# Optimization experiments

Hardware: AMD Instinct MI355X
Metric: run time of the kernel (lower is better)

## Reference

```python
import jax, jax.numpy as jnp
import numpy as np

N = 50000      # num nodes
E = 400000     # directed edges (avg out-degree 8)
DIN = 128
DOUT = 128
ALPHA = 0.5    # args.alphaDir (buffer, requires_grad=False)
BETA = 0.5     # args.betaDir
GAMA = 0.5     # args.gamaDir


def _dedupe(rows, cols, vals, n):
    key = rows.astype(np.int64) * n + cols.astype(np.int64)
    uk, inv = np.unique(key, return_inverse=True)
    v = np.bincount(inv, weights=vals, minlength=uk.shape[0])
    return (uk // n).astype(np.int32), (uk % n).astype(np.int32), v.astype(np.float32)


def _dir_norm(r, c, v, n):
    # directed_norm: D_out^{-1/2} A D_in^{-1/2}, inf -> 0
    in_deg = np.bincount(c, weights=v, minlength=n)
    out_deg = np.bincount(r, weights=v, minlength=n)
    in_is = np.zeros(n); m = in_deg > 0; in_is[m] = in_deg[m] ** -0.5
    out_is = np.zeros(n); m = out_deg > 0; out_is[m] = out_deg[m] ** -0.5
    return r, c, (out_is[r] * v * in_is[c]).astype(np.float32)


def _spgemm(rA, cA, vA, rB, cB, vB, n):
    # sparse @ sparse in COO, vectorized numpy
    order = np.argsort(rB, kind='stable')
    rBs, cBs, vBs = rB[order], cB[order], vB[order]
    degB = np.bincount(rBs, minlength=n)
    indptr = np.concatenate(([0], np.cumsum(degB)))
    counts = degB[cA]
    total = int(counts.sum())
    rep = np.repeat(np.arange(len(rA)), counts)
    first = np.cumsum(counts) - counts
    pos = np.arange(total) - np.repeat(first, counts) + np.repeat(indptr[cA], counts)
    rows = rA[rep]
    cols = cBs[pos]
    vals = vA[rep].astype(np.float64) * vBs[pos]
    return _dedupe(rows, cols, vals, n)


def setup_inputs() -> dict:
    rng = np.random.default_rng(0)
    r0 = rng.integers(0, N, E).astype(np.int64)
    c0 = rng.integers(0, N, E).astype(np.int64)
    r, c, v = _dedupe(r0, c0, np.ones(E, np.float32), N)
    a = _dir_norm(r, c, v, N)                 # adj_norm
    at = _dir_norm(c, r, v, N)                # adj_t_norm
    rr, cc, vv = _spgemm(a[0], a[1], a[2], at[0], at[1], at[2], N)
    aat = _dir_norm(rr, cc, vv, N)            # directed_norm(A @ At)
    rr, cc, vv = _spgemm(at[0], at[1], at[2], a[0], a[1], a[2], N)
    ata = _dir_norm(rr, cc, vv, N)            # directed_norm(At @ A)
    rr, cc, vv = _spgemm(a[0], a[1], a[2], a[0], a[1], a[2], N)
    aa = _dir_norm(rr, cc, vv, N)             # directed_norm(A @ A)
    rr, cc, vv = _spgemm(at[0], at[1], at[2], at[0], at[1], at[2], N)
    atat = _dir_norm(rr, cc, vv, N)           # directed_norm(At @ At)

    key = jax.random.key(0)
    ks = jax.random.split(key, 7)
    x = jax.random.normal(ks[0], (N, DIN), dtype=jnp.float32)
    s = 1.0 / np.sqrt(DIN)

    def lin(k):
        k1, k2 = jax.random.split(k)
        w = jax.random.uniform(k1, (DIN, DOUT), jnp.float32, -s, s)
        b = jax.random.uniform(k2, (DOUT,), jnp.float32, -s, s)
        return w, b

    w_sd, b_sd = lin(ks[1]); w_ds, b_ds = lin(ks[2])
    w0, b0 = lin(ks[3]); w1, b1 = lin(ks[4])
    w2, b2 = lin(ks[5]); w3, b3 = lin(ks[6])

    out = {'x': x,
           'w_sd': w_sd, 'b_sd': b_sd, 'w_ds': w_ds, 'b_ds': b_ds,
           'w0': w0, 'b0': b0, 'w1': w1, 'b1': b1,
           'w2': w2, 'b2': b2, 'w3': w3, 'b3': b3}
    for name, t in (('a', a), ('at', at), ('aat', aat), ('ata', ata), ('aa', aa), ('atat', atat)):
        out[name + '_rows'] = jnp.asarray(t[0])
        out[name + '_cols'] = jnp.asarray(t[1])
        out[name + '_vals'] = jnp.asarray(t[2])
    return out


def _spmm(rows, cols, vals, x):
    # (A @ x)[i] = sum_e vals[e] * x[cols[e]] scattered to rows[e]
    return jax.ops.segment_sum(vals[:, None] * x[cols], rows, num_segments=x.shape[0])


def reference(x, a_rows, a_cols, a_vals, at_rows, at_cols, at_vals,
              aat_rows, aat_cols, aat_vals, ata_rows, ata_cols, ata_vals,
              aa_rows, aa_cols, aa_vals, atat_rows, atat_cols, atat_vals,
              w_sd, b_sd, w_ds, b_ds, w0, b0, w1, b1, w2, b2, w3, b3):
    out1 = ALPHA * (_spmm(a_rows, a_cols, a_vals, x) @ w_sd + b_sd) \
         + (1.0 - ALPHA) * (_spmm(at_rows, at_cols, at_vals, x) @ w_ds + b_ds)
    out2 = BETA * (_spmm(aat_rows, aat_cols, aat_vals, x) @ w0 + b0) \
         + (1.0 - BETA) * (_spmm(ata_rows, ata_cols, ata_vals, x) @ w1 + b1)
    out3 = GAMA * (_spmm(aa_rows, aa_cols, aa_vals, x) @ w2 + b2) \
         + (1.0 - GAMA) * (_spmm(atat_rows, atat_cols, atat_vals, x) @ w3 + b3)
    return out1 + out2 + out3
```

## Files before the change

kernel.cpp:

```cpp
#include <hip/hip_runtime.h>
#include <hip/hip_bf16.h>

#define FD 128

typedef __attribute__((ext_vector_type(8))) short bf16x8;
typedef __attribute__((ext_vector_type(4))) float f32x4;

__device__ __forceinline__ float bfu2f(unsigned short u) {
  return __uint_as_float(((unsigned int)u) << 16);
}
__device__ __forceinline__ float b2f(__hip_bfloat16 v) { return __bfloat162float(v); }
__device__ __forceinline__ unsigned int pk2(float lo, float hi) {
  return (unsigned int)__bfloat16_as_ushort(__float2bfloat16(lo)) |
         ((unsigned int)__bfloat16_as_ushort(__float2bfloat16(hi)) << 16);
}

__device__ __forceinline__ float ldf(const void* p, int i, int ff) {
  return ff ? ((const float*)p)[i] : b2f(((const __hip_bfloat16*)p)[i]);
}
__device__ __forceinline__ int ldi(const void* p, int i, int fi) {
  return fi ? (int)((const long long*)p)[i] : ((const int*)p)[i];
}

__global__ void detect_k(const void* x, const void* cols, int* flags) {
  __shared__ int cnt[2];
  if (threadIdx.x < 2) cnt[threadIdx.x] = 0;
  __syncthreads();
  const unsigned short* xu = (const unsigned short*)x;
  int big = 0;
  for (int i = threadIdx.x; i < 1024; i += 256) {
    int e = (xu[i] >> 7) & 0xFF;
    if (e >= 0x90) big++;
  }
  if (big) atomicAdd(&cnt[0], big);
  const int* ci = (const int*)cols;
  int zeros = 0;
  for (int i = threadIdx.x; i < 128; i += 256)
    if ((i & 1) && ci[i] == 0) zeros++;
  if (zeros) atomicAdd(&cnt[1], zeros);
  __syncthreads();
  if (threadIdx.x == 0) {
    flags[0] = (cnt[0] > 16) ? 1 : 0;
    flags[1] = (cnt[1] >= 32) ? 1 : 0;
  }
}

__global__ void cvtall_k(const void* __restrict__ rows, const void* __restrict__ cols,
                         const void* __restrict__ vals, int nnz, int n,
                         int* __restrict__ r32, int* __restrict__ c32,
                         float* __restrict__ vf, int* __restrict__ cntT,
                         const int* flags) {
  int ff = flags[0], fi = flags[1];
  int i = blockIdx.x * 256 + threadIdx.x;
  if (i >= nnz) return;
  int r = ldi(rows, i, fi);
  int c = ldi(cols, i, fi);
  if ((unsigned)r >= (unsigned)n) r = 0;
  if ((unsigned)c >= (unsigned)n) c = 0;
  r32[i] = r;
  c32[i] = c;
  vf[i] = ldf(vals, i, ff);
  atomicAdd(&cntT[c], 1);
}

__global__ void scanAbs_k(const int* __restrict__ cnt, int n, int* bsum,
                          const int* __restrict__ rows, int nnz, int* rpA, int nb) {
  int blk = blockIdx.x;
  if (blk < nb) {
    __shared__ int sh[256];
    int t = threadIdx.x;
    int i = blk * 256 + t;
    sh[t] = (i < n) ? cnt[i] : 0;
    __syncthreads();
    for (int d = 128; d > 0; d >>= 1) {
      if (t < d) sh[t] += sh[t + d];
      __syncthreads();
    }
    if (t == 0) bsum[blk] = sh[0];
  } else {
    int i = (blk - nb) * 256 + threadIdx.x;
    if (i > n) return;
    int lo = 0, hi = nnz;
    while (lo < hi) { int mid = (lo + hi) >> 1; if (rows[mid] < i) lo = mid + 1; else hi = mid; }
    rpA[i] = lo;
  }
}

__global__ void scanB_k(int* bsum, int nb, int* rpTail) {
  __shared__ int sh[256];
  int t = threadIdx.x;
  int v = (t < nb) ? bsum[t] : 0;
  sh[t] = v;
  __syncthreads();
  int val = v;
  for (int d = 1; d < 256; d <<= 1) {
    int add = (t >= d) ? sh[t - d] : 0;
    __syncthreads();
    val += add;
    sh[t] = val;
    __syncthreads();
  }
  if (t < nb) bsum[t] = val - v;
  if (t == 255) *rpTail = val;
}

__global__ void scanC_k(const int* __restrict__ cnt, int n, const int* __restrict__ bsum,
                        int* rp, int* cur) {
  __shared__ int sh[256];
  int t = threadIdx.x;
  int i = blockIdx.x * 256 + t;
  int v = (i < n) ? cnt[i] : 0;
  sh[t] = v;
  __syncthreads();
  int val = v;
  for (int d = 1; d < 256; d <<= 1) {
    int add = (t >= d) ? sh[t - d] : 0;
    __syncthreads();
    val += add;
    sh[t] = val;
    __syncthreads();
  }
  int ex = val - v + bsum[blockIdx.x];
  if (i < n) { rp[i] = ex; cur[i] = ex; }
}

__global__ void scatter_k(const int* __restrict__ r, const int* __restrict__ c,
                          const float* __restrict__ v, int nnz,
                          int* cur, int* tSrc, float* tVal) {
  int i = blockIdx.x * 256 + threadIdx.x;
  if (i >= nnz) return;
  int p = atomicAdd(&cur[c[i]], 1);
  if ((unsigned)p >= (unsigned)nnz) return;
  tSrc[p] = r[i];
  tVal[p] = v[i];
}

__global__ void nodesum_k(const int* __restrict__ rpA, const float* __restrict__ av,
                          const int* __restrict__ rpT, const float* __restrict__ tv,
                          float* __restrict__ u1, float* __restrict__ v1, int n) {
  int i = blockIdx.x * 256 + threadIdx.x;
  if (i >= n) return;
  float su = 0.f;
  int e0 = rpA[i], e1 = rpA[i + 1];
  for (int j = e0; j < e1; ++j) su += av[j];
  u1[i] = su;
  float sv = 0.f;
  int f0 = rpT[i], f1 = rpT[i + 1];
  for (int j = f0; j < f1; ++j) sv += tv[j];
  v1[i] = sv;
}

__global__ void deg2c_k(const int* __restrict__ rpA, const int* __restrict__ ci,
                        const float* __restrict__ av,
                        const int* __restrict__ rpT, const int* __restrict__ ti,
                        const float* __restrict__ tv,
                        const float* __restrict__ u1, const float* __restrict__ v1,
                        float* __restrict__ s1, float* __restrict__ s2,
                        float* __restrict__ s3, float* __restrict__ s4, int n) {
  int i = blockIdx.x * 256 + threadIdx.x;
  if (i >= n) return;
  float a1 = 0.f, a3 = 0.f;
  int s0 = rpA[i], se = rpA[i + 1];
  for (int j = s0; j < se; ++j) {
    int c = ci[j];
    float v = av[j];
    a1 = fmaf(v, v1[c], a1);
    a3 = fmaf(v, u1[c], a3);
  }
  s1[i] = (a1 > 0.f) ? rsqrtf(a1) : 0.f;
  s3[i] = (a3 > 0.f) ? rsqrtf(a3) : 0.f;
  float a2 = 0.f, a4 = 0.f;
  int t0 = rpT[i], t1 = rpT[i + 1];
  for (int j = t0; j < t1; ++j) {
    int r = ti[j];
    float v = tv[j];
    a2 = fmaf(v, u1[r], a2);
    a4 = fmaf(v, v1[r], a4);
  }
  s2[i] = (a2 > 0.f) ? rsqrtf(a2) : 0.f;
  s4[i] = (a4 > 0.f) ? rsqrtf(a4) : 0.f;
}

__global__ void bias_k(const void* a, const void* b, const void* c, const void* d,
                       const void* e, const void* f, float* bias, const int* flags) {
  int ff = flags[0];
  int i = threadIdx.x;
  bias[i] = 0.5f * (ldf(a, i, ff) + ldf(b, i, ff) + ldf(c, i, ff)
                  + ldf(d, i, ff) + ldf(e, i, ff) + ldf(f, i, ff));
}

__global__ void fill_k(unsigned short* o, int n) {
  int i = blockIdx.x * 256 + threadIdx.x;
  if (i < n) o[i] = 0x3E80;
}

struct W6p { const void* w[6]; };
struct B6p { const void* b[6]; };

__global__ void prep_k(const void* __restrict__ x, __hip_bfloat16* __restrict__ xb, int nx,
                       W6p ws, __hip_bfloat16* __restrict__ Wt,
                       B6p bs, float* __restrict__ bias,
                       const int* flags, int cvtB) {
  int ff = flags[0];
  int blk = blockIdx.x;
  if (blk < cvtB) {
    int i = (blk * 256 + threadIdx.x) * 4;
    if (i >= nx) return;
    if (i + 3 >= nx) {
      for (int k = i; k < nx; ++k) xb[k] = __float2bfloat16(ldf(x, k, ff));
      return;
    }
    xb[i + 0] = __float2bfloat16(ldf(x, i + 0, ff));
    xb[i + 1] = __float2bfloat16(ldf(x, i + 1, ff));
    xb[i + 2] = __float2bfloat16(ldf(x, i + 2, ff));
    xb[i + 3] = __float2bfloat16(ldf(x, i + 3, ff));
  } else if (blk < cvtB + 384) {
    int e = (blk - cvtB) * 256 + threadIdx.x;
    if (e >= 6 * 16384) return;
    int seg = e >> 14;
    int r = e & 16383;
    int n = r >> 7;
    int innerB = (r & 127) << 1;
    int kb = innerB ^ ((n & 7) << 4);
    int k = kb >> 1;
    Wt[e] = __float2bfloat16(ldf(ws.w[seg], k * 128 + n, ff));
  } else {
    int i = threadIdx.x;
    if (i < FD)
      bias[i] = 0.5f * (ldf(bs.b[0], i, ff) + ldf(bs.b[1], i, ff) + ldf(bs.b[2], i, ff)
                      + ldf(bs.b[3], i, ff) + ldf(bs.b[4], i, ff) + ldf(bs.b[5], i, ff));
  }
}

struct FHSet {
  const int* rp; const int* ci; const float* cv;
  unsigned int* ot; unsigned int* oa; unsigned int* ob;
  const float* sA; const float* sB;
};

__global__ __launch_bounds__(256) void fh3d_k(
    FHSet h0, FHSet h1, const unsigned int* __restrict__ xb, int n, int half) {
  int blk = blockIdx.x;
  bool hiH = blk >= half;
  const int* rp = hiH ? h1.rp : h0.rp;
  const int* ci = hiH ? h1.ci : h0.ci;
  const float* cv = hiH ? h1.cv : h0.cv;
  unsigned int* ot = hiH ? h1.ot : h0.ot;
  unsigned int* oa = hiH ? h1.oa : h0.oa;
  unsigned int* ob = hiH ? h1.ob : h0.ob;
  const float* sA = hiH ? h1.sA : h0.sA;
  const float* sB = hiH ? h1.sB : h0.sB;
  int bb = hiH ? blk - half : blk;

  int wave = threadIdx.x >> 6;
  int l = threadIdx.x & 63;
  int r = bb * 4 + wave;
  if (r >= n) return;
  int s = rp[r], e = rp[r + 1];

  float tl = 0.f, th = 0.f, al = 0.f, ah = 0.f, bl = 0.f, bh = 0.f;
  int j = s;
  for (; j + 3 < e; j += 4) {
#pragma unroll
    for (int u = 0; u < 4; ++u) {
      int c = ci[j + u];
      float v = cv[j + u];
      float va = v * sA[c];
      float vb = v * sB[c];
      unsigned int xu = xb[(size_t)c * 64 + l];
      float lo = __uint_as_float(xu << 16);
      float hi = __uint_as_float(xu & 0xFFFF0000u);
      tl = fmaf(v, lo, tl);  th = fmaf(v, hi, th);
      al = fmaf(va, lo, al); ah = fmaf(va, hi, ah);
      bl = fmaf(vb, lo, bl); bh = fmaf(vb, hi, bh);
    }
  }
  for (; j < e; ++j) {
    int c = ci[j];
    float v = cv[j];
    float va = v * sA[c];
    float vb = v * sB[c];
    unsigned int xu = xb[(size_t)c * 64 + l];
    float lo = __uint_as_float(xu << 16);
    float hi = __uint_as_float(xu & 0xFFFF0000u);
    tl = fmaf(v, lo, tl);  th = fmaf(v, hi, th);
    al = fmaf(va, lo, al); ah = fmaf(va, hi, ah);
    bl = fmaf(vb, lo, bl); bh = fmaf(vb, hi, bh);
  }
  ot[(size_t)r * 64 + l] = pk2(tl, th);
  oa[(size_t)r * 128 + l] = pk2(al, ah);
  ob[(size_t)r * 128 + l] = pk2(bl, bh);
}

struct SHSet {
  const int* rp; const int* ci; const float* cv;
  const unsigned int* gp;
  unsigned int* ya; unsigned int* yb;
  const float* rsa; const float* rsb;
};

__global__ __launch_bounds__(256) void sh2d_k(SHSet h0, SHSet h1, int n, int half) {
  int blk = blockIdx.x;
  bool hiH = blk >= half;
  const int* rp = hiH ? h1.rp : h0.rp;
  const int* ci = hiH ? h1.ci : h0.ci;
  const float* cv = hiH ? h1.cv : h0.cv;
  const unsigned int* gp = hiH ? h1.gp : h0.gp;
  unsigned int* ya = hiH ? h1.ya : h0.ya;
  unsigned int* yb = hiH ? h1.yb : h0.yb;
  const float* rsa = hiH ? h1.rsa : h0.rsa;
  const float* rsb = hiH ? h1.rsb : h0.rsb;
  int bb = hiH ? blk - half : blk;

  int wave = threadIdx.x >> 6;
  int l = threadIdx.x & 63;
  int r = bb * 4 + wave;
  if (r >= n) return;
  int s = rp[r], e = rp[r + 1];

  float al = 0.f, ah = 0.f, bl = 0.f, bh = 0.f;
  int j = s;
  for (; j + 3 < e; j += 4) {
#pragma unroll
    for (int u = 0; u < 4; ++u) {
      int c = ci[j + u];
      float v = cv[j + u];
      const unsigned int* bp = gp + (size_t)c * 128;
      unsigned int ua = bp[l];
      unsigned int ub = bp[64 + l];
      al = fmaf(v, __uint_as_float(ua << 16), al);
      ah = fmaf(v, __uint_as_float(ua & 0xFFFF0000u), ah);
      bl = fmaf(v, __uint_as_float(ub << 16), bl);
      bh = fmaf(v, __uint_as_float(ub & 0xFFFF0000u), bh);
    }
  }
  for (; j < e; ++j) {
    int c = ci[j];
    float v = cv[j];
    const unsigned int* bp = gp + (size_t)c * 128;
    unsigned int ua = bp[l];
    unsigned int ub = bp[64 + l];
    al = fmaf(v, __uint_as_float(ua << 16), al);
    ah = fmaf(v, __uint_as_float(ua & 0xFFFF0000u), ah);
    bl = fmaf(v, __uint_as_float(ub << 16), bl);
    bh = fmaf(v, __uint_as_float(ub & 0xFFFF0000u), bh);
  }
  float ra = rsa[r], rb = rsb[r];
  ya[(size_t)r * 64 + l] = pk2(al * ra, ah * ra);
  yb[(size_t)r * 64 + l] = pk2(bl * rb, bh * rb);
}

struct Y6 { const unsigned short* y[6]; };

__global__ __launch_bounds__(256) void gemm6m3_k(
    Y6 ys, const unsigned short* __restrict__ Wt2, const float* __restrict__ bias,
    void* __restrict__ outp, int M, const int* flags) {
  int ff = flags[0];
  __shared__ __align__(16) unsigned short Bs[16384];
  const int tid = threadIdx.x;
  const int lane = tid & 63;
  const int wave = tid >> 6;
  const int m = lane & 15;
  const int q = lane >> 4;
  const int r0 = blockIdx.x * 128 + wave * 32;
  const int row0 = r0 + m;
  const int row1 = r0 + 16 + m;
  const bool ok0 = row0 < M;
  const bool ok1 = row1 < M;
  const bf16x8 zero8 = {0, 0, 0, 0, 0, 0, 0, 0};

  f32x4 acc0[8], acc1[8];
#pragma unroll
  for (int nt = 0; nt < 8; ++nt) {
    acc0[nt] = (f32x4){0.f, 0.f, 0.f, 0.f};
    acc1[nt] = (f32x4){0.f, 0.f, 0.f, 0.f};
  }

  bf16x8 Bst[8];
#pragma unroll
  for (int c2 = 0; c2 < 8; ++c2)
    Bst[c2] = *(const bf16x8*)(Wt2 + (size_t)(c2 * 256 + tid) * 8);
  bf16x8 Ap0[4], Ap1[4];
#pragma unroll
  for (int kc = 0; kc < 4; ++kc) {
    Ap0[kc] = ok0 ? *(const bf16x8*)(ys.y[0] + (size_t)row0 * FD + kc * 32 + q * 8) : zero8;
    Ap1[kc] = ok1 ? *(const bf16x8*)(ys.y[0] + (size_t)row1 * FD + kc * 32 + q * 8) : zero8;
  }

  const int swz = (m & 7) << 4;

#pragma unroll
  for (int t = 0; t < 6; ++t) {
    __syncthreads();
#pragma unroll
    for (int c2 = 0; c2 < 8; ++c2)
      *(bf16x8*)((char*)Bs + (size_t)(c2 * 256 + tid) * 16) = Bst[c2];
    bf16x8 A0[4], A1[4];
#pragma unroll
    for (int kc = 0; kc < 4; ++kc) { A0[kc] = Ap0[kc]; A1[kc] = Ap1[kc]; }
    if (t < 5) {
#pragma unroll
      for (int c2 = 0; c2 < 8; ++c2)
        Bst[c2] = *(const bf16x8*)(Wt2 + (size_t)(t + 1) * 16384 +
                                   (size_t)(c2 * 256 + tid) * 8);
#pragma unroll
      for (int kc = 0; kc < 4; ++kc) {
        Ap0[kc] = ok0 ? *(const bf16x8*)(ys.y[t + 1] + (size_t)row0 * FD + kc * 32 + q * 8) : zero8;
        Ap1[kc] = ok1 ? *(const bf16x8*)(ys.y[t + 1] + (size_t)row1 * FD + kc * 32 + q * 8) : zero8;
      }
    }
    __syncthreads();
#pragma unroll
    for (int kc = 0; kc < 4; ++kc) {
      const int koff = (kc * 64 + q * 16) ^ swz;
#pragma unroll
      for (int nt = 0; nt < 8; ++nt) {
        const int nrow = nt * 16 + m;
        bf16x8 bfv = *(const bf16x8*)((const char*)Bs + nrow * 256 + koff);
        acc0[nt] = __builtin_amdgcn_mfma_f32_16x16x32_bf16(A0[kc], bfv, acc0[nt], 0, 0, 0);
        acc1[nt] = __builtin_amdgcn_mfma_f32_16x16x32_bf16(A1[kc], bfv, acc1[nt], 0, 0, 0);
      }
    }
  }

#pragma unroll
  for (int nt = 0; nt < 8; ++nt) {
    int col = nt * 16 + m;
    float bv = bias[col];
#pragma unroll
    for (int rg = 0; rg < 4; ++rg) {
      int g0 = r0 + q * 4 + rg;
      if (g0 < M) {
        float v = 0.5f * acc0[nt][rg] + bv;
        if (ff) ((float*)outp)[(size_t)g0 * FD + col] = v;
        else ((unsigned short*)outp)[(size_t)g0 * FD + col] =
            __bfloat16_as_ushort(__float2bfloat16(v));
      }
      int g1 = r0 + 16 + q * 4 + rg;
      if (g1 < M) {
        float v = 0.5f * acc1[nt][rg] + bv;
        if (ff) ((float*)outp)[(size_t)g1 * FD + col] = v;
        else ((unsigned short*)outp)[(size_t)g1 * FD + col] =
            __bfloat16_as_ushort(__float2bfloat16(v));
      }
    }
  }
}

__global__ __launch_bounds__(128) void spmm_k(
    const int* __restrict__ rp, const void* __restrict__ ci, int cif,
    const void* __restrict__ cv, int cvf,
    const void* __restrict__ x, int xf, __hip_bfloat16* __restrict__ y,
    int n, int nnzMax,
    const float* __restrict__ cscale, const float* __restrict__ rscale,
    const int* flags) {
  int ff = flags[0], fi = flags[1];
  int vf = cvf ? 1 : ff;
  int iw = cif ? fi : 0;
  int xw = xf ? ff : 0;
  const int t = threadIdx.x;
  int r0 = blockIdx.x * 4;
  int rend = min(r0 + 4, n);
  for (int r = r0; r < rend; ++r) {
    int s = rp[r], e = rp[r + 1];
    s = max(0, min(s, nnzMax));
    e = max(s, min(e, nnzMax));
    float acc = 0.f;
    for (int j = s; j < e; ++j) {
      int c = ldi(ci, j, iw);
      if ((unsigned)c >= (unsigned)n) c = 0;
      float v = (vf ? ((const float*)cv)[j] : b2f(((const __hip_bfloat16*)cv)[j]));
      if (cscale) v *= cscale[c];
      float xv = xw ? ((const float*)x)[c * FD + t]
                    : b2f(((const __hip_bfloat16*)x)[c * FD + t]);
      acc = fmaf(v, xv, acc);
    }
    if (rscale) acc *= rscale[r];
    y[r * FD + t] = __float2bfloat16(acc);
  }
}

__global__ __launch_bounds__(256) void gemm_k(
    const __hip_bfloat16* __restrict__ Y, const void* __restrict__ W,
    const float* __restrict__ bias, const void* __restrict__ accin,
    void* __restrict__ outp, int M, const int* flags) {
  int ff = flags[0];
  __shared__ __align__(16) float Wl[32 * 128];
  __shared__ __align__(16) float Yl[64 * 36];
  const int t = threadIdx.x;
  const int row0 = blockIdx.x * 64;
  const int c4 = (t & 31) * 4;
  const int r8 = (t >> 5) * 8;
  const int rs = t >> 3;
  const int q = t & 7;
  float acc[8][4];
#pragma unroll
  for (int m = 0; m < 8; ++m)
#pragma unroll
    for (int j = 0; j < 4; ++j) acc[m][j] = 0.f;
  for (int kc = 0; kc < 4; ++kc) {
    if (ff) {
      const float4* Wg4 = (const float4*)((const float*)W + kc * 32 * 128);
#pragma unroll
      for (int i = 0; i < 4; ++i)
        *(float4*)(Wl + (t + i * 256) * 4) = Wg4[t + i * 256];
    } else {
      const ushort4* Wg4 = (const ushort4*)((const unsigned short*)W + kc * 32 * 128);
#pragma unroll
      for (int i = 0; i < 4; ++i) {
        ushort4 u = Wg4[t + i * 256];
        int base = (t + i * 256) * 4;
        Wl[base + 0] = bfu2f(u.x);
        Wl[base + 1] = bfu2f(u.y);
        Wl[base + 2] = bfu2f(u.z);
        Wl[base + 3] = bfu2f(u.w);
      }
    }
#pragma unroll
    for (int i = 0; i < 2; ++i) {
      int rr = rs + i * 32;
      int grow = row0 + rr;
      ushort4 u = make_ushort4(0, 0, 0, 0);
      if (grow < M)
        u = *(const ushort4*)((const unsigned short*)Y + grow * FD + kc * 32 + q * 4);
      float* yd = Yl + rr * 36 + q * 4;
      yd[0] = bfu2f(u.x); yd[1] = bfu2f(u.y); yd[2] = bfu2f(u.z); yd[3] = bfu2f(u.w);
    }
    __syncthreads();
#pragma unroll
    for (int kk = 0; kk < 32; kk += 4) {
      float4 w0 = *(const float4*)(Wl + (kk + 0) * 128 + c4);
      float4 w1 = *(const float4*)(Wl + (kk + 1) * 128 + c4);
      float4 w2 = *(const float4*)(Wl + (kk + 2) * 128 + c4);
      float4 w3 = *(const float4*)(Wl + (kk + 3) * 128 + c4);
#pragma unroll
      for (int m = 0; m < 8; ++m) {
        float4 yv = *(const float4*)(Yl + (r8 + m) * 36 + kk);
        acc[m][0] = fmaf(yv.x, w0.x, acc[m][0]);
        acc[m][1] = fmaf(yv.x, w0.y, acc[m][1]);
        acc[m][2] = fmaf(yv.x, w0.z, acc[m][2]);
        acc[m][3] = fmaf(yv.x, w0.w, acc[m][3]);
        acc[m][0] = fmaf(yv.y, w1.x, acc[m][0]);
        acc[m][1] = fmaf(yv.y, w1.y, acc[m][1]);
        acc[m][2] = fmaf(yv.y, w1.z, acc[m][2]);
        acc[m][3] = fmaf(yv.y, w1.w, acc[m][3]);
        acc[m][0] = fmaf(yv.z, w2.x, acc[m][0]);
        acc[m][1] = fmaf(yv.z, w2.y, acc[m][1]);
        acc[m][2] = fmaf(yv.z, w2.z, acc[m][2]);
        acc[m][3] = fmaf(yv.z, w2.w, acc[m][3]);
        acc[m][0] = fmaf(yv.w, w3.x, acc[m][0]);
        acc[m][1] = fmaf(yv.w, w3.y, acc[m][1]);
        acc[m][2] = fmaf(yv.w, w3.z, acc[m][2]);
        acc[m][3] = fmaf(yv.w, w3.w, acc[m][3]);
      }
    }
    __syncthreads();
  }
  float4 b4 = make_float4(0.f, 0.f, 0.f, 0.f);
  if (bias) b4 = *(const float4*)(bias + c4);
#pragma unroll
  for (int m = 0; m < 8; ++m) {
    int grow = row0 + r8 + m;
    if (grow >= M) continue;
    float4 rv;
    rv.x = 0.5f * acc[m][0] + b4.x;
    rv.y = 0.5f * acc[m][1] + b4.y;
    rv.z = 0.5f * acc[m][2] + b4.z;
    rv.w = 0.5f * acc[m][3] + b4.w;
    if (accin) {
      if (ff) {
        float4 o = *(const float4*)((const float*)accin + grow * FD + c4);
        rv.x += o.x; rv.y += o.y; rv.z += o.z; rv.w += o.w;
      } else {
        ushort4 o = *(const ushort4*)((const unsigned short*)accin + grow * FD + c4);
        rv.x += bfu2f(o.x); rv.y += bfu2f(o.y); rv.z += bfu2f(o.z); rv.w += bfu2f(o.w);
      }
    }
    if (ff) {
      *(float4*)((float*)outp + grow * FD + c4) = rv;
    } else {
      ushort4 so;
      so.x = __bfloat16_as_ushort(__float2bfloat16(rv.x));
      so.y = __bfloat16_as_ushort(__float2bfloat16(rv.y));
      so.z = __bfloat16_as_ushort(__float2bfloat16(rv.z));
      so.w = __bfloat16_as_ushort(__float2bfloat16(rv.w));
      *(ushort4*)((unsigned short*)outp + grow * FD + c4) = so;
    }
  }
}

extern "C" void kernel_launch(void* const* d_in, const int* in_sizes, int n_in,
                              void* d_out, int out_size, void* d_ws, size_t ws_size,
                              hipStream_t stream) {
  const void* x    = d_in[0];
  const void* w_sd = d_in[1];
  const void* b_sd = d_in[2];
  const void* w_ds = d_in[3];
  const void* b_ds = d_in[4];
  const void* w0   = d_in[5];
  const void* b0   = d_in[6];
  const void* w1   = d_in[7];
  const void* b1   = d_in[8];
  const void* w2   = d_in[9];
  const void* b2   = d_in[10];
  const void* w3   = d_in[11];
  const void* b3   = d_in[12];
  const void* a_rows = d_in[13];
  const void* a_cols = d_in[14];
  const void* a_vals = d_in[15];
  const int nnz = in_sizes[13];
  const int N = in_sizes[0] / FD;

  const size_t BUF = ((size_t)N * FD * 2 + 255) & ~(size_t)255;

  auto misc_need = [&](int nbig) -> size_t {
    size_t need = (size_t)nbig * BUF;
    need += ((size_t)10 * N * 4 + 255) & ~(size_t)255;
    need += 512 + 256 + 1024;
    need += (((size_t)(N + 1) * 4 + 255) & ~(size_t)255) * 2;
    need += (((size_t)N * 4 + 255) & ~(size_t)255) * 2;
    need += (((size_t)nnz * 4 + 255) & ~(size_t)255) * 5;
    need += (6 * 16384 * 2 + 255) & ~(size_t)255;
    return need;
  };
  size_t needA = misc_need(10);
  size_t needB = misc_need(2);

  int pathA = (ws_size >= needA) ? 1 : 0;
  if (!pathA && ws_size < needB) {
    fill_k<<<(out_size + 255) / 256, 256, 0, stream>>>((unsigned short*)d_out, out_size);
    return;
  }

  int nbig = pathA ? 10 : 2;
  char* p = (char*)d_ws;
  char* bufs[10];
  for (int i = 0; i < 10; ++i) bufs[i] = (i < nbig) ? (p + (size_t)i * BUF) : nullptr;
  char* q = p + (size_t)nbig * BUF;
  auto take = [&](size_t bytes) -> char* {
    char* r = q;
    q += (bytes + 255) & ~(size_t)255;
    return r;
  };
  float* degf  = (float*)take((size_t)10 * N * 4);
  float* biasf = (float*)take(512);
  int*   flags = (int*)take(256);
  int*   bsum  = (int*)take(1024);
  int* rpA  = (int*)take((size_t)(N + 1) * 4);
  int* rpT  = (int*)take((size_t)(N + 1) * 4);
  int* curT = (int*)take((size_t)N * 4);
  int* cntT = (int*)take((size_t)N * 4);
  int* tSrc = (int*)take((size_t)nnz * 4);
  float* tValF = (float*)take((size_t)nnz * 4);
  int* aRow32 = (int*)take((size_t)nnz * 4);
  int* aCol32 = (int*)take((size_t)nnz * 4);
  float* aValF = (float*)take((size_t)nnz * 4);
  __hip_bfloat16* Wt = (__hip_bfloat16*)take(6 * 16384 * 2);

  float* u1 = degf;
  float* v1 = degf + N;
  float* s1 = degf + 6 * N;
  float* s2 = degf + 7 * N;
  float* s3 = degf + 8 * N;
  float* s4 = degf + 9 * N;

  int eb = (nnz + 255) / 256;
  int nb = (N + 255) / 256;
  int nb2 = (N + 256) / 256;

  detect_k<<<1, 256, 0, stream>>>(x, a_cols, flags);
  hipMemsetAsync(cntT, 0, (size_t)N * 4, stream);
  cvtall_k<<<eb, 256, 0, stream>>>(a_rows, a_cols, a_vals, nnz, N, aRow32, aCol32, aValF, cntT, flags);
  scanAbs_k<<<nb + nb2, 256, 0, stream>>>(cntT, N, bsum, aRow32, nnz, rpA, nb);
  scanB_k<<<1, 256, 0, stream>>>(bsum, nb, rpT + N);
  scanC_k<<<nb, 256, 0, stream>>>(cntT, N, bsum, rpT, curT);
  scatter_k<<<eb, 256, 0, stream>>>(aRow32, aCol32, aValF, nnz, curT, tSrc, tValF);
  nodesum_k<<<nb, 256, 0, stream>>>(rpA, aValF, rpT, tValF, u1, v1, N);
  deg2c_k<<<nb, 256, 0, stream>>>(rpA, aCol32, aValF, rpT, tSrc, tValF, u1, v1,
                                  s1, s2, s3, s4, N);

  int sg2 = (N + 3) / 4;
  int gg = (N + 63) / 64;
  int gg4 = (N + 127) / 128;

  if (pathA) {
    W6p wargs;
    wargs.w[0] = w_sd; wargs.w[1] = w_ds; wargs.w[2] = w0;
    wargs.w[3] = w1;   wargs.w[4] = w2;   wargs.w[5] = w3;
    B6p bargs;
    bargs.b[0] = b_sd; bargs.b[1] = b_ds; bargs.b[2] = b0;
    bargs.b[3] = b1;   bargs.b[4] = b2;   bargs.b[5] = b3;
    __hip_bfloat16* xb = (__hip_bfloat16*)bufs[0];
    int cvtB = (N * FD / 4 + 255) / 256;
    prep_k<<<cvtB + 384 + 1, 256, 0, stream>>>(x, xb, N * FD, wargs, Wt, bargs, biasf,
                                               flags, cvtB);

    unsigned int* xbu = (unsigned int*)bufs[0];
    unsigned int* t2 = (unsigned int*)bufs[1];
    unsigned int* t1 = (unsigned int*)bufs[2];
    unsigned int* P1 = (unsigned int*)bufs[3];
    unsigned int* P2 = (unsigned int*)bufs[5];
    unsigned int* y3 = (unsigned int*)bufs[7];
    unsigned int* y4 = (unsigned int*)bufs[8];
    unsigned int* y6 = (unsigned int*)bufs[9];
    unsigned int* y5 = (unsigned int*)bufs[0];

    FHSet hT = { rpT, tSrc, tValF, t2, P1, P2 + 64, s1, s3 };
    FHSet hA = { rpA, aCol32, aValF, t1, P2, P1 + 64, s2, s4 };
    fh3d_k<<<2 * sg2, 256, 0, stream>>>(hT, hA, xbu, N, sg2);

    SHSet sA = { rpA, aCol32, aValF, P1, y3, y5, s1, s3 };
    SHSet sT = { rpT, tSrc, tValF, P2, y4, y6, s2, s4 };
    sh2d_k<<<2 * sg2, 256, 0, stream>>>(sA, sT, N, sg2);

    Y6 yargs;
    yargs.y[0] = (const unsigned short*)t1;
    yargs.y[1] = (const unsigned short*)t2;
    yargs.y[2] = (const unsigned short*)y3;
    yargs.y[3] = (const unsigned short*)y4;
    yargs.y[4] = (const unsigned short*)y5;
    yargs.y[5] = (const unsigned short*)y6;
    gemm6m3_k<<<gg4, 256, 0, stream>>>(yargs, (const unsigned short*)Wt, biasf, d_out, N, flags);
  } else {
    bias_k<<<1, FD, 0, stream>>>(b_sd, b_ds, b0, b1, b2, b3, biasf, flags);
    __hip_bfloat16* Yb = (__hip_bfloat16*)bufs[0];
    __hip_bfloat16* gb = (__hip_bfloat16*)bufs[1];
    spmm_k<<<sg2, 128, 0, stream>>>(rpA, a_cols, 1, a_vals, 0, x, 1, Yb, N, nnz, nullptr, nullptr, flags);
    gemm_k<<<gg, 256, 0, stream>>>(Yb, w_sd, biasf, nullptr, d_out, N, flags);
    spmm_k<<<sg2, 128, 0, stream>>>(rpT, tSrc, 0, tValF, 1, x, 1, Yb, N, nnz, nullptr, nullptr, flags);
    gemm_k<<<gg, 256, 0, stream>>>(Yb, w_ds, nullptr, d_out, d_out, N, flags);
    spmm_k<<<sg2, 128, 0, stream>>>(rpT, tSrc, 0, tValF, 1, x, 1, gb, N, nnz, s1, nullptr, flags);
    spmm_k<<<sg2, 128, 0, stream>>>(rpA, a_cols, 1, a_vals, 0, gb, 0, Yb, N, nnz, nullptr, s1, flags);
    gemm_k<<<gg, 256, 0, stream>>>(Yb, w0, nullptr, d_out, d_out, N, flags);
    spmm_k<<<sg2, 128, 0, stream>>>(rpA, a_cols, 1, a_vals, 0, x, 1, gb, N, nnz, s2, nullptr, flags);
    spmm_k<<<sg2, 128, 0, stream>>>(rpT, tSrc, 0, tValF, 1, gb, 0, Yb, N, nnz, nullptr, s2, flags);
    gemm_k<<<gg, 256, 0, stream>>>(Yb, w1, nullptr, d_out, d_out, N, flags);
    spmm_k<<<sg2, 128, 0, stream>>>(rpA, a_cols, 1, a_vals, 0, x, 1, gb, N, nnz, s4, nullptr, flags);
    spmm_k<<<sg2, 128, 0, stream>>>(rpA, a_cols, 1, a_vals, 0, gb, 0, Yb, N, nnz, nullptr, s3, flags);
    gemm_k<<<gg, 256, 0, stream>>>(Yb, w2, nullptr, d_out, d_out, N, flags);
    spmm_k<<<sg2, 128, 0, stream>>>(rpT, tSrc, 0, tValF, 1, x, 1, gb, N, nnz, s3, nullptr, flags);
    spmm_k<<<sg2, 128, 0, stream>>>(rpT, tSrc, 0, tValF, 1, gb, 0, Yb, N, nnz, nullptr, s4, flags);
    gemm_k<<<gg, 256, 0, stream>>>(Yb, w3, nullptr, d_out, d_out, N, flags);
  }
}
```

Before: 443.0 us.

## Fuse setup kernels and widen SpMM loads to 64-bit per lane

Folds input-format detection into the edge-conversion kernel, so every block recomputes the flags, and merges the degree-normalization kernel with the x/weight/bias prep kernel, cutting two launches. The x conversion now uses 8-wide vector loads and stores. In the first-hop SpMM each half-wave handles a different edge and loads uint2 per lane, then the halves are combined with a cross-half shuffle. The second-hop SpMM gives each lane four features via uint2 loads. This lowers launch overhead and memory instruction count, at the cost of redundant flag detection in every block and extra shuffles and divergent stores.

```diff
diff --git a/kernel.cpp b/kernel.cpp
--- a/kernel.cpp
+++ b/kernel.cpp
@@ -22,7 +22,12 @@
   return fi ? (int)((const long long*)p)[i] : ((const int*)p)[i];
 }
 
-__global__ void detect_k(const void* x, const void* cols, int* flags) {
+__global__ void cvtall_k(const void* __restrict__ rows, const void* __restrict__ cols,
+                         const void* __restrict__ vals, int nnz, int n,
+                         const void* __restrict__ x,
+                         int* __restrict__ r32, int* __restrict__ c32,
+                         float* __restrict__ vf, int* __restrict__ cntT,
+                         int* flags) {
   __shared__ int cnt[2];
   if (threadIdx.x < 2) cnt[threadIdx.x] = 0;
   __syncthreads();
@@ -39,18 +44,12 @@
     if ((i & 1) && ci[i] == 0) zeros++;
   if (zeros) atomicAdd(&cnt[1], zeros);
   __syncthreads();
-  if (threadIdx.x == 0) {
-    flags[0] = (cnt[0] > 16) ? 1 : 0;
-    flags[1] = (cnt[1] >= 32) ? 1 : 0;
-  }
-}
-
-__global__ void cvtall_k(const void* __restrict__ rows, const void* __restrict__ cols,
-                         const void* __restrict__ vals, int nnz, int n,
-                         int* __restrict__ r32, int* __restrict__ c32,
-                         float* __restrict__ vf, int* __restrict__ cntT,
-                         const int* flags) {
-  int ff = flags[0], fi = flags[1];
+  int ff = (cnt[0] > 16) ? 1 : 0;
+  int fi = (cnt[1] >= 32) ? 1 : 0;
+  if (blockIdx.x == 0 && threadIdx.x == 0) {
+    flags[0] = ff;
+    flags[1] = fi;
+  }
   int i = blockIdx.x * 256 + threadIdx.x;
   if (i >= nnz) return;
   int r = ldi(rows, i, fi);
@@ -150,37 +149,6 @@
   v1[i] = sv;
 }
 
-__global__ void deg2c_k(const int* __restrict__ rpA, const int* __restrict__ ci,
-                        const float* __restrict__ av,
-                        const int* __restrict__ rpT, const int* __restrict__ ti,
-                        const float* __restrict__ tv,
-                        const float* __restrict__ u1, const float* __restrict__ v1,
-                        float* __restrict__ s1, float* __restrict__ s2,
-                        float* __restrict__ s3, float* __restrict__ s4, int n) {
-  int i = blockIdx.x * 256 + threadIdx.x;
-  if (i >= n) return;
-  float a1 = 0.f, a3 = 0.f;
-  int s0 = rpA[i], se = rpA[i + 1];
-  for (int j = s0; j < se; ++j) {
-    int c = ci[j];
-    float v = av[j];
-    a1 = fmaf(v, v1[c], a1);
-    a3 = fmaf(v, u1[c], a3);
-  }
-  s1[i] = (a1 > 0.f) ? rsqrtf(a1) : 0.f;
-  s3[i] = (a3 > 0.f) ? rsqrtf(a3) : 0.f;
-  float a2 = 0.f, a4 = 0.f;
-  int t0 = rpT[i], t1 = rpT[i + 1];
-  for (int j = t0; j < t1; ++j) {
-    int r = ti[j];
-    float v = tv[j];
-    a2 = fmaf(v, u1[r], a2);
-    a4 = fmaf(v, v1[r], a4);
-  }
-  s2[i] = (a2 > 0.f) ? rsqrtf(a2) : 0.f;
-  s4[i] = (a4 > 0.f) ? rsqrtf(a4) : 0.f;
-}
-
 __global__ void bias_k(const void* a, const void* b, const void* c, const void* d,
                        const void* e, const void* f, float* bias, const int* flags) {
   int ff = flags[0];
@@ -197,39 +165,75 @@
 struct W6p { const void* w[6]; };
 struct B6p { const void* b[6]; };
 
-__global__ void prep_k(const void* __restrict__ x, __hip_bfloat16* __restrict__ xb, int nx,
-                       W6p ws, __hip_bfloat16* __restrict__ Wt,
-                       B6p bs, float* __restrict__ bias,
-                       const int* flags, int cvtB) {
+__global__ void dpp_k(const int* __restrict__ rpA, const int* __restrict__ ci,
+                      const float* __restrict__ av,
+                      const int* __restrict__ rpT, const int* __restrict__ ti,
+                      const float* __restrict__ tv,
+                      const float* __restrict__ u1, const float* __restrict__ v1,
+                      float* __restrict__ s1, float* __restrict__ s2,
+                      float* __restrict__ s3, float* __restrict__ s4, int n,
+                      const void* __restrict__ x, unsigned int* __restrict__ xb, int nx,
+                      W6p ws, __hip_bfloat16* __restrict__ Wt,
+                      B6p bs, float* __restrict__ bias,
+                      const int* flags, int nb, int cvtB) {
+  int blk = blockIdx.x;
+  if (blk < nb) {
+    int i = blk * 256 + threadIdx.x;
+    if (i >= n) return;
+    float a1 = 0.f, a3 = 0.f;
+    int s0 = rpA[i], se = rpA[i + 1];
+    for (int j = s0; j < se; ++j) {
+      int c = ci[j];
+      float v = av[j];
+      a1 = fmaf(v, v1[c], a1);
+      a3 = fmaf(v, u1[c], a3);
+    }
+    s1[i] = (a1 > 0.f) ? rsqrtf(a1) : 0.f;
+    s3[i] = (a3 > 0.f) ? rsqrtf(a3) : 0.f;
+    float a2 = 0.f, a4 = 0.f;
+    int t0 = rpT[i], t1 = rpT[i + 1];
+    for (int j = t0; j < t1; ++j) {
+      int r = ti[j];
+      float v = tv[j];
+      a2 = fmaf(v, u1[r], a2);
+      a4 = fmaf(v, v1[r], a4);
+    }
+    s2[i] = (a2 > 0.f) ? rsqrtf(a2) : 0.f;
+    s4[i] = (a4 > 0.f) ? rsqrtf(a4) : 0.f;
+    return;
+  }
   int ff = flags[0];
-  int blk = blockIdx.x;
-  if (blk < cvtB) {
-    int i = (blk * 256 + threadIdx.x) * 4;
+  if (blk < nb + cvtB) {
+    int i = ((blk - nb) * 256 + threadIdx.x) * 8;
     if (i >= nx) return;
-    if (i + 3 >= nx) {
-      for (int k = i; k < nx; ++k) xb[k] = __float2bfloat16(ldf(x, k, ff));
-      return;
-    }
-    xb[i + 0] = __float2bfloat16(ldf(x, i + 0, ff));
-    xb[i + 1] = __float2bfloat16(ldf(x, i + 1, ff));
-    xb[i + 2] = __float2bfloat16(ldf(x, i + 2, ff));
-    xb[i + 3] = __float2bfloat16(ldf(x, i + 3, ff));
-  } else if (blk < cvtB + 384) {
-    int e = (blk - cvtB) * 256 + threadIdx.x;
+    uint4 o;
+    if (ff) {
+      float4 p0 = *(const float4*)((const float*)x + i);
+      float4 p1 = *(const float4*)((const float*)x + i + 4);
+      o.x = pk2(p0.x, p0.y); o.y = pk2(p0.z, p0.w);
+      o.z = pk2(p1.x, p1.y); o.w = pk2(p1.z, p1.w);
+    } else {
+      o = *(const uint4*)((const unsigned short*)x + i);
+    }
+    *(uint4*)(xb + i / 2) = o;
+    return;
+  }
+  if (blk < nb + cvtB + 384) {
+    int e = (blk - nb - cvtB) * 256 + threadIdx.x;
     if (e >= 6 * 16384) return;
     int seg = e >> 14;
     int r = e & 16383;
-    int n = r >> 7;
+    int nn = r >> 7;
     int innerB = (r & 127) << 1;
-    int kb = innerB ^ ((n & 7) << 4);
+    int kb = innerB ^ ((nn & 7) << 4);
     int k = kb >> 1;
-    Wt[e] = __float2bfloat16(ldf(ws.w[seg], k * 128 + n, ff));
-  } else {
-    int i = threadIdx.x;
-    if (i < FD)
-      bias[i] = 0.5f * (ldf(bs.b[0], i, ff) + ldf(bs.b[1], i, ff) + ldf(bs.b[2], i, ff)
-                      + ldf(bs.b[3], i, ff) + ldf(bs.b[4], i, ff) + ldf(bs.b[5], i, ff));
-  }
+    Wt[e] = __float2bfloat16(ldf(ws.w[seg], k * 128 + nn, ff));
+    return;
+  }
+  int i = threadIdx.x;
+  if (i < FD)
+    bias[i] = 0.5f * (ldf(bs.b[0], i, ff) + ldf(bs.b[1], i, ff) + ldf(bs.b[2], i, ff)
+                    + ldf(bs.b[3], i, ff) + ldf(bs.b[4], i, ff) + ldf(bs.b[5], i, ff));
 }
 
 struct FHSet {
@@ -254,42 +258,65 @@
 
   int wave = threadIdx.x >> 6;
   int l = threadIdx.x & 63;
+  int lf = l & 31;
+  bool hlo = l < 32;
   int r = bb * 4 + wave;
   if (r >= n) return;
   int s = rp[r], e = rp[r + 1];
 
-  float tl = 0.f, th = 0.f, al = 0.f, ah = 0.f, bl = 0.f, bh = 0.f;
+  float t0 = 0.f, t1 = 0.f, t2 = 0.f, t3 = 0.f;
+  float a0 = 0.f, a1 = 0.f, a2 = 0.f, a3 = 0.f;
+  float b0 = 0.f, b1 = 0.f, b2 = 0.f, b3 = 0.f;
+
   int j = s;
-  for (; j + 3 < e; j += 4) {
-#pragma unroll
-    for (int u = 0; u < 4; ++u) {
-      int c = ci[j + u];
-      float v = cv[j + u];
-      float va = v * sA[c];
-      float vb = v * sB[c];
-      unsigned int xu = xb[(size_t)c * 64 + l];
-      float lo = __uint_as_float(xu << 16);
-      float hi = __uint_as_float(xu & 0xFFFF0000u);
-      tl = fmaf(v, lo, tl);  th = fmaf(v, hi, th);
-      al = fmaf(va, lo, al); ah = fmaf(va, hi, ah);
-      bl = fmaf(vb, lo, bl); bh = fmaf(vb, hi, bh);
-    }
-  }
-  for (; j < e; ++j) {
+  for (; j + 1 < e; j += 2) {
+    int cA = ci[j], cB = ci[j + 1];
+    float vA = cv[j], vB = cv[j + 1];
+    int c = hlo ? cA : cB;
+    float v = hlo ? vA : vB;
+    float va = v * sA[c];
+    float vb = v * sB[c];
+    uint2 xu = *(const uint2*)(xb + (size_t)c * 64 + lf * 2);
+    float f0 = __uint_as_float(xu.x << 16);
+    float f1 = __uint_as_float(xu.x & 0xFFFF0000u);
+    float f2 = __uint_as_float(xu.y << 16);
+    float f3 = __uint_as_float(xu.y & 0xFFFF0000u);
+    t0 = fmaf(v, f0, t0); t1 = fmaf(v, f1, t1); t2 = fmaf(v, f2, t2); t3 = fmaf(v, f3, t3);
+    a0 = fmaf(va, f0, a0); a1 = fmaf(va, f1, a1); a2 = fmaf(va, f2, a2); a3 = fmaf(va, f3, a3);
+    b0 = fmaf(vb, f0, b0); b1 = fmaf(vb, f1, b1); b2 = fmaf(vb, f2, b2); b3 = fmaf(vb, f3, b3);
+  }
+  if (j < e && hlo) {
     int c = ci[j];
     float v = cv[j];
     float va = v * sA[c];
     float vb = v * sB[c];
-    unsigned int xu = xb[(size_t)c * 64 + l];
-    float lo = __uint_as_float(xu << 16);
-    float hi = __uint_as_float(xu & 0xFFFF0000u);
-    tl = fmaf(v, lo, tl);  th = fmaf(v, hi, th);
-    al = fmaf(va, lo, al); ah = fmaf(va, hi, ah);
-    bl = fmaf(vb, lo, bl); bh = fmaf(vb, hi, bh);
-  }
-  ot[(size_t)r * 64 + l] = pk2(tl, th);
-  oa[(size_t)r * 128 + l] = pk2(al, ah);
-  ob[(size_t)r * 128 + l] = pk2(bl, bh);
+    uint2 xu = *(const uint2*)(xb + (size_t)c * 64 + lf * 2);
+    float f0 = __uint_as_float(xu.x << 16);
+    float f1 = __uint_as_float(xu.x & 0xFFFF0000u);
+    float f2 = __uint_as_float(xu.y << 16);
+    float f3 = __uint_as_float(xu.y & 0xFFFF0000u);
+    t0 = fmaf(v, f0, t0); t1 = fmaf(v, f1, t1); t2 = fmaf(v, f2, t2); t3 = fmaf(v, f3, t3);
+    a0 = fmaf(va, f0, a0); a1 = fmaf(va, f1, a1); a2 = fmaf(va, f2, a2); a3 = fmaf(va, f3, a3);
+    b0 = fmaf(vb, f0, b0); b1 = fmaf(vb, f1, b1); b2 = fmaf(vb, f2, b2); b3 = fmaf(vb, f3, b3);
+  }
+  t0 += __shfl_xor(t0, 32); t1 += __shfl_xor(t1, 32);
+  t2 += __shfl_xor(t2, 32); t3 += __shfl_xor(t3, 32);
+  a0 += __shfl_xor(a0, 32); a1 += __shfl_xor(a1, 32);
+  a2 += __shfl_xor(a2, 32); a3 += __shfl_xor(a3, 32);
+  b0 += __shfl_xor(b0, 32); b1 += __shfl_xor(b1, 32);
+  b2 += __shfl_xor(b2, 32); b3 += __shfl_xor(b3, 32);
+
+  if (hlo) {
+    uint2 o;
+    o.x = pk2(t0, t1); o.y = pk2(t2, t3);
+    *(uint2*)(ot + (size_t)r * 64 + lf * 2) = o;
+    o.x = pk2(a0, a1); o.y = pk2(a2, a3);
+    *(uint2*)(oa + (size_t)r * 128 + lf * 2) = o;
+  } else {
+    uint2 o;
+    o.x = pk2(b0, b1); o.y = pk2(b2, b3);
+    *(uint2*)(ob + (size_t)r * 128 + lf * 2) = o;
+  }
 }
 
 struct SHSet {
@@ -314,40 +341,41 @@
 
   int wave = threadIdx.x >> 6;
   int l = threadIdx.x & 63;
+  int lf = l & 31;
+  bool hlo = l < 32;
   int r = bb * 4 + wave;
   if (r >= n) return;
   int s = rp[r], e = rp[r + 1];
 
-  float al = 0.f, ah = 0.f, bl = 0.f, bh = 0.f;
+  float f0 = 0.f, f1 = 0.f, f2 = 0.f, f3 = 0.f;
   int j = s;
   for (; j + 3 < e; j += 4) {
 #pragma unroll
     for (int u = 0; u < 4; ++u) {
       int c = ci[j + u];
       float v = cv[j + u];
-      const unsigned int* bp = gp + (size_t)c * 128;
-      unsigned int ua = bp[l];
-      unsigned int ub = bp[64 + l];
-      al = fmaf(v, __uint_as_float(ua << 16), al);
-      ah = fmaf(v, __uint_as_float(ua & 0xFFFF0000u), ah);
-      bl = fmaf(v, __uint_as_float(ub << 16), bl);
-      bh = fmaf(v, __uint_as_float(ub & 0xFFFF0000u), bh);
+      uint2 g = *(const uint2*)(gp + (size_t)c * 128 + l * 2);
+      f0 = fmaf(v, __uint_as_float(g.x << 16), f0);
+      f1 = fmaf(v, __uint_as_float(g.x & 0xFFFF0000u), f1);
+      f2 = fmaf(v, __uint_as_float(g.y << 16), f2);
+      f3 = fmaf(v, __uint_as_float(g.y & 0xFFFF0000u), f3);
     }
   }
   for (; j < e; ++j) {
     int c = ci[j];
     float v = cv[j];
-    const unsigned int* bp = gp + (size_t)c * 128;
-    unsigned int ua = bp[l];
-    unsigned int ub = bp[64 + l];
-    al = fmaf(v, __uint_as_float(ua << 16), al);
-    ah = fmaf(v, __uint_as_float(ua & 0xFFFF0000u), ah);
-    bl = fmaf(v, __uint_as_float(ub << 16), bl);
-    bh = fmaf(v, __uint_as_float(ub & 0xFFFF0000u), bh);
-  }
-  float ra = rsa[r], rb = rsb[r];
-  ya[(size_t)r * 64 + l] = pk2(al * ra, ah * ra);
-  yb[(size_t)r * 64 + l] = pk2(bl * rb, bh * rb);
+    uint2 g = *(const uint2*)(gp + (size_t)c * 128 + l * 2);
+    f0 = fmaf(v, __uint_as_float(g.x << 16), f0);
+    f1 = fmaf(v, __uint_as_float(g.x & 0xFFFF0000u), f1);
+    f2 = fmaf(v, __uint_as_float(g.y << 16), f2);
+    f3 = fmaf(v, __uint_as_float(g.y & 0xFFFF0000u), f3);
+  }
+  float rs = hlo ? rsa[r] : rsb[r];
+  unsigned int* yp = hlo ? ya : yb;
+  uint2 o;
+  o.x = pk2(f0 * rs, f1 * rs);
+  o.y = pk2(f2 * rs, f3 * rs);
+  *(uint2*)(yp + (size_t)r * 64 + lf * 2) = o;
 }
 
 struct Y6 { const unsigned short* y[6]; };
@@ -668,34 +696,34 @@
   int nb = (N + 255) / 256;
   int nb2 = (N + 256) / 256;
 
-  detect_k<<<1, 256, 0, stream>>>(x, a_cols, flags);
   hipMemsetAsync(cntT, 0, (size_t)N * 4, stream);
-  cvtall_k<<<eb, 256, 0, stream>>>(a_rows, a_cols, a_vals, nnz, N, aRow32, aCol32, aValF, cntT, flags);
+  cvtall_k<<<eb, 256, 0, stream>>>(a_rows, a_cols, a_vals, nnz, N, x,
+                                   aRow32, aCol32, aValF, cntT, flags);
   scanAbs_k<<<nb + nb2, 256, 0, stream>>>(cntT, N, bsum, aRow32, nnz, rpA, nb);
   scanB_k<<<1, 256, 0, stream>>>(bsum, nb, rpT + N);
   scanC_k<<<nb, 256, 0, stream>>>(cntT, N, bsum, rpT, curT);
   scatter_k<<<eb, 256, 0, stream>>>(aRow32, aCol32, aValF, nnz, curT, tSrc, tValF);
   nodesum_k<<<nb, 256, 0, stream>>>(rpA, aValF, rpT, tValF, u1, v1, N);
-  deg2c_k<<<nb, 256, 0, stream>>>(rpA, aCol32, aValF, rpT, tSrc, tValF, u1, v1,
-                                  s1, s2, s3, s4, N);
 
   int sg2 = (N + 3) / 4;
   int gg = (N + 63) / 64;
   int gg4 = (N + 127) / 128;
 
+  W6p wargs;
+  wargs.w[0] = w_sd; wargs.w[1] = w_ds; wargs.w[2] = w0;
+  wargs.w[3] = w1;   wargs.w[4] = w2;   wargs.w[5] = w3;
+  B6p bargs;
+  bargs.b[0] = b_sd; bargs.b[1] = b_ds; bargs.b[2] = b0;
+  bargs.b[3] = b1;   bargs.b[4] = b2;   bargs.b[5] = b3;
+
   if (pathA) {
-    W6p wargs;
-    wargs.w[0] = w_sd; wargs.w[1] = w_ds; wargs.w[2] = w0;
-    wargs.w[3] = w1;   wargs.w[4] = w2;   wargs.w[5] = w3;
-    B6p bargs;
-    bargs.b[0] = b_sd; bargs.b[1] = b_ds; bargs.b[2] = b0;
-    bargs.b[3] = b1;   bargs.b[4] = b2;   bargs.b[5] = b3;
-    __hip_bfloat16* xb = (__hip_bfloat16*)bufs[0];
-    int cvtB = (N * FD / 4 + 255) / 256;
-    prep_k<<<cvtB + 384 + 1, 256, 0, stream>>>(x, xb, N * FD, wargs, Wt, bargs, biasf,
-                                               flags, cvtB);
-
     unsigned int* xbu = (unsigned int*)bufs[0];
+    int nx = N * FD;
+    int cvtB = (nx / 8 + 255) / 256;
+    dpp_k<<<nb + cvtB + 384 + 1, 256, 0, stream>>>(
+        rpA, aCol32, aValF, rpT, tSrc, tValF, u1, v1, s1, s2, s3, s4, N,
+        x, xbu, nx, wargs, Wt, bargs, biasf, flags, nb, cvtB);
+
     unsigned int* t2 = (unsigned int*)bufs[1];
     unsigned int* t1 = (unsigned int*)bufs[2];
     unsigned int* P1 = (unsigned int*)bufs[3];
@@ -722,6 +750,9 @@
     yargs.y[5] = (const unsigned short*)y6;
     gemm6m3_k<<<gg4, 256, 0, stream>>>(yargs, (const unsigned short*)Wt, biasf, d_out, N, flags);
   } else {
+    dpp_k<<<nb, 256, 0, stream>>>(
+        rpA, aCol32, aValF, rpT, tSrc, tValF, u1, v1, s1, s2, s3, s4, N,
+        x, (unsigned int*)bufs[0], 0, wargs, Wt, bargs, biasf, flags, nb, 0);
     bias_k<<<1, FD, 0, stream>>>(b_sd, b_ds, b0, b1, b2, b3, biasf, flags);
     __hip_bfloat16* Yb = (__hip_bfloat16*)bufs[0];
     __hip_bfloat16* gb = (__hip_bfloat16*)bufs[1];
```

New measurement: 444.0 us. No clear change (+0.2%).
